# Performance work log

Measured on AMD Instinct MI355X. Metric: run time of the kernel, lower is better.

The kernel has to match this reference:

```python
import jax, jax.numpy as jnp
import numpy as np

INPUT_SIZE = 8
HIDDEN = 64


def setup_inputs() -> dict:
    key = jax.random.key(0)
    ks = jax.random.split(key, 7)
    B, T = 4096, 512
    s_ih = 1.0 / np.sqrt(HIDDEN)
    return {
        "input": jax.random.normal(ks[0], (B, T, INPUT_SIZE), dtype=jnp.float32),
        # PyTorch LSTM params: gate order i, f, g, o stacked along dim 0
        "W_ih": jax.random.uniform(ks[1], (4 * HIDDEN, INPUT_SIZE), minval=-s_ih, maxval=s_ih, dtype=jnp.float32),
        "W_hh": jax.random.uniform(ks[2], (4 * HIDDEN, HIDDEN), minval=-s_ih, maxval=s_ih, dtype=jnp.float32),
        "b_ih": jax.random.uniform(ks[3], (4 * HIDDEN,), minval=-s_ih, maxval=s_ih, dtype=jnp.float32),
        "b_hh": jax.random.uniform(ks[4], (4 * HIDDEN,), minval=-s_ih, maxval=s_ih, dtype=jnp.float32),
        "W_dense": jax.random.uniform(ks[5], (1, HIDDEN), minval=-s_ih, maxval=s_ih, dtype=jnp.float32),
        "b_dense": jax.random.uniform(ks[6], (1,), minval=-s_ih, maxval=s_ih, dtype=jnp.float32),
    }


def _lstm_seq(x, W_ih, W_hh, b_ih, b_hh):
    # x: [B, T, I] -> h_seq: [B, T, H]
    B = x.shape[0]
    # precompute input projections for all timesteps: [T, B, 4H]
    x_proj = jnp.einsum('bti,gi->tbg', x, W_ih) + (b_ih + b_hh)

    def step(carry, xp):
        h, c = carry
        gates = xp + h @ W_hh.T  # [B, 4H]
        i, f, g, o = jnp.split(gates, 4, axis=-1)
        i = jax.nn.sigmoid(i)
        f = jax.nn.sigmoid(f)
        g = jnp.tanh(g)
        o = jax.nn.sigmoid(o)
        c = f * c + i * g
        h = o * jnp.tanh(c)
        return (h, c), h

    h0 = jnp.zeros((B, HIDDEN), dtype=x.dtype)
    c0 = jnp.zeros((B, HIDDEN), dtype=x.dtype)
    _, h_seq = jax.lax.scan(step, (h0, c0), x_proj)  # [T, B, H]
    return jnp.transpose(h_seq, (1, 0, 2))  # [B, T, H]


def reference(input, W_ih, W_hh, b_ih, b_hh, W_dense, b_dense):
    h_t = _lstm_seq(input, W_ih, W_hh, b_ih, b_hh)  # [B, T, H]
    return h_t @ W_dense.T + b_dense  # [B, T, 1]
```

## Files before the change

### kernel.cpp

```cpp
#include <hip/hip_runtime.h>

#define T_SEQ 512
#define ISZ 8
#define HID 64
#define L2E 1.44269504088896340736f

typedef __bf16 bf16x8 __attribute__((ext_vector_type(8)));
typedef float  f32x4  __attribute__((ext_vector_type(4)));

__device__ __forceinline__ float exp2_hw(float x) {
    float r; asm("v_exp_f32 %0, %1" : "=v"(r) : "v"(x)); return r;
}
__device__ __forceinline__ unsigned cvt_pk_bf16(float a, float b) {
    unsigned r; asm("v_cvt_pk_bf16_f32 %0, %1, %2" : "=v"(r) : "v"(a), "v"(b)); return r;
}

__global__ __launch_bounds__(256, 2) void lstm_v7_kernel(
    const float* __restrict__ x,
    const float* __restrict__ W_ih,
    const float* __restrict__ W_hh,
    const float* __restrict__ b_ih,
    const float* __restrict__ b_hh,
    const float* __restrict__ W_dense,
    const float* __restrict__ b_dense,
    float* __restrict__ out)
{
    __shared__ __align__(16) __bf16 hpl[2][16 * 64];
    __shared__ __align__(16) __bf16 xs[2][160];
    __shared__ __align__(16) __bf16 xz[8];

    const int tid  = threadIdx.x;
    const int lane = tid & 63;
    const int w    = tid >> 6;
    const int q    = lane >> 4;
    const int sub  = lane & 15;
    const int br   = 2 * (sub >> 2) + (sub & 1);
    const bool isLo = (sub & 2) != 0;
    const long b0  = (long)blockIdx.x * 8;

    bf16x8 Bg[4][3];
    float biasg[4];
    #pragma unroll
    for (int g = 0; g < 4; ++g) {
        const int m = g * HID + 16 * w + sub;
        const float sc = (g == 2) ? (2.0f * L2E) : (-L2E);
        biasg[g] = (b_ih[m] + b_hh[m]) * sc;
        #pragma unroll
        for (int s = 0; s < 3; ++s) {
            #pragma unroll
            for (int e = 0; e < 8; ++e) {
                const int k = 32 * s + 8 * q + e;
                float v = 0.0f;
                if (k < HID)            v = W_hh[m * HID + k] * sc;
                else if (k < HID + ISZ) v = W_ih[m * ISZ + (k - HID)] * sc;
                Bg[g][s][e] = (__bf16)v;
            }
        }
    }
    f32x4 Cs[4];
    #pragma unroll
    for (int g = 0; g < 4; ++g) { Cs[g][0] = biasg[g]; Cs[g][1] = biasg[g]; Cs[g][2] = 0.f; Cs[g][3] = 0.f; }

    bf16x8 Bwd[2];
    #pragma unroll
    for (int s = 0; s < 2; ++s) {
        #pragma unroll
        for (int e = 0; e < 8; ++e) {
            const int k = 32 * s + 8 * q + e;
            const float wv = W_dense[k];
            const __bf16 whi = (__bf16)wv;
            float val = (sub == 0) ? (float)whi : (sub == 1) ? (wv - (float)whi) : 0.0f;
            Bwd[s][e] = (__bf16)val;
        }
    }

    for (int i = tid; i < 512; i += 256) ((float*)&hpl[1][0])[i] = 0.0f;
    if (tid < 4) ((float*)&xz[0])[tid] = 0.0f;

    const int  pr = lane >> 1, ph = lane & 1;
    const float* xbase = x + ((b0 + pr) * (long)T_SEQ) * ISZ + ph * 4;
    const int  xoffH = pr * 8 + ph * 4;
    const int  xoffL = 64 + xoffH;

    if (w == 3 && lane < 16) {
        float4 xv = *(const float4*)xbase;
        unsigned h01 = cvt_pk_bf16(xv.x, xv.y);
        unsigned h23 = cvt_pk_bf16(xv.z, xv.w);
        float f0 = __uint_as_float(h01 << 16), f1 = __uint_as_float(h01 & 0xffff0000u);
        float f2 = __uint_as_float(h23 << 16), f3 = __uint_as_float(h23 & 0xffff0000u);
        unsigned l01 = cvt_pk_bf16(xv.x - f0, xv.y - f1);
        unsigned l23 = cvt_pk_bf16(xv.z - f2, xv.w - f3);
        uint2 hh2; hh2.x = h01; hh2.y = h23;
        uint2 ll2; ll2.x = l01; ll2.y = l23;
        *(uint2*)&xs[0][xoffH] = hh2;
        *(uint2*)&xs[0][xoffL] = ll2;
    }

    const __bf16* xrd0 = (q == 0) ? &xs[0][(isLo ? 64 : 0) + br * 8] : &xz[0];
    const __bf16* xrd1 = (q == 0) ? &xs[1][(isLo ? 64 : 0) + br * 8] : &xz[0];

    float c0 = 0.f, c1 = 0.f;
    const float bd  = b_dense[0];
    const f32x4 Z   = {0.f, 0.f, 0.f, 0.f};
    const int  swz  = (sub & 7) << 3;
    const int  jme  = 16 * w + sub;

    float s0[4], s1[4];
    s0[0]=s0[1]=s0[2]=s0[3]=0.f;
    s1[0]=s1[1]=s1[2]=s1[3]=0.f;

    __syncthreads();

#define MF(A, B, C) __builtin_amdgcn_mfma_f32_16x16x32_bf16(A, B, C, 0, 0, 0)

#define STEP(P, PB, XR, XW)                                                          \
    {                                                                                \
        const int t = tb + P;                                                        \
                    \
        float4 xv;                                                                   \
        if (w == 3 && lane < 16) {                                                   \
            const int tn = (t + 1 < T_SEQ) ? (t + 1) : (T_SEQ - 1);                  \
            xv = *(const float4*)(xbase + (long)tn * ISZ);                           \
        }                                                                            \
            \
        bf16x8 Ax  = *(const bf16x8*)(XR);                                           \
        bf16x8 Ah0 = *(const bf16x8*)&hpl[PB][sub * 64 + ((8 * q)      ^ swz)];      \
        bf16x8 Ah1 = *(const bf16x8*)&hpl[PB][sub * 64 + ((32 + 8 * q) ^ swz)];      \
                                            \
        __builtin_amdgcn_s_setprio(1);                                               \
        f32x4 a0 = MF(Ax, Bg[0][2], Cs[0]);                                          \
        f32x4 a1 = MF(Ax, Bg[1][2], Cs[1]);                                          \
        f32x4 a2 = MF(Ax, Bg[2][2], Cs[2]);                                          \
        f32x4 a3 = MF(Ax, Bg[3][2], Cs[3]);                                          \
        a0 = MF(Ah0, Bg[0][0], a0); a0 = MF(Ah1, Bg[0][1], a0);                      \
        a1 = MF(Ah0, Bg[1][0], a1); a1 = MF(Ah1, Bg[1][1], a1);                      \
        a2 = MF(Ah0, Bg[2][0], a2); a2 = MF(Ah1, Bg[2][1], a2);                      \
        a3 = MF(Ah0, Bg[3][0], a3); a3 = MF(Ah1, Bg[3][1], a3);                      \
        __builtin_amdgcn_s_setprio(0);                                               \
                                 \
        if (w == 0) {                                                                \
            f32x4 oz = MF(Ah0, Bwd[0], Z);                                           \
            oz = MF(Ah1, Bwd[1], oz);                                                \
            float v0 = oz[0] + oz[2];                                                \
            float v1 = oz[1] + oz[3];                                                \
            v0 += __shfl_xor(v0, 1);                                                 \
            v1 += __shfl_xor(v1, 1);                                                 \
            s0[(P + 3) & 3] = v0;                                                    \
            s1[(P + 3) & 3] = v1;                                                    \
        }                                                                            \
                   \
        _Pragma("unroll")                                                            \
        for (int i = 0; i < 2; ++i) {                                                \
            const float gi = a0[i] + a0[2 + i];                                      \
            const float gf = a1[i] + a1[2 + i];                                      \
            const float gg = a2[i] + a2[2 + i];                                      \
            const float go = a3[i] + a3[2 + i];                                      \
            const float eA = exp2_hw(gi);                                            \
            const float eF = exp2_hw(gf);                                            \
            const float eB = exp2_hw(gg);                                            \
            const float ig = (eB - 1.0f) *                                           \
                __builtin_amdgcn_rcpf((1.0f + eA) * (1.0f + eB));                    \
            const float ff = __builtin_amdgcn_rcpf(1.0f + eF);                       \
            float cc = i ? c1 : c0;                                                  \
            cc = fmaf(ff, cc, ig);                                                   \
            if (i) c1 = cc; else c0 = cc;                                            \
            const float eO = exp2_hw(go);                                            \
            const float eC = exp2_hw(fminf(cc * (2.0f * L2E), 80.0f));               \
            const float hh = (eC - 1.0f) *                                           \
                __builtin_amdgcn_rcpf((1.0f + eO) * (1.0f + eC));                    \
            const __bf16 hi = (__bf16)hh;                                            \
            const __bf16 lo = (__bf16)(hh - (float)hi);                              \
            const int rh = 4 * q + i;                                                \
            const int rl = rh + 2;                                                   \
            hpl[PB ^ 1][rh * 64 + (jme ^ ((rh & 7) << 3))] = hi;                     \
            hpl[PB ^ 1][rl * 64 + (jme ^ ((rl & 7) << 3))] = lo;                     \
        }                                                                            \
               \
        if (w == 3 && lane < 16) {                                                   \
            unsigned h01 = cvt_pk_bf16(xv.x, xv.y);                                  \
            unsigned h23 = cvt_pk_bf16(xv.z, xv.w);                                  \
            float f0 = __uint_as_float(h01 << 16);                                   \
            float f1 = __uint_as_float(h01 & 0xffff0000u);                           \
            float f2 = __uint_as_float(h23 << 16);                                   \
            float f3 = __uint_as_float(h23 & 0xffff0000u);                           \
            unsigned l01 = cvt_pk_bf16(xv.x - f0, xv.y - f1);                        \
            unsigned l23 = cvt_pk_bf16(xv.z - f2, xv.w - f3);                        \
            uint2 hh2; hh2.x = h01; hh2.y = h23;                                     \
            uint2 ll2; ll2.x = l01; ll2.y = l23;                                     \
            *(uint2*)&xs[XW][xoffH] = hh2;                                           \
            *(uint2*)&xs[XW][xoffL] = ll2;                                           \
        }                                                                            \
                 \
        if (P == 0) {                                                                \
            if (w == 0 && sub == 0 && tb >= 4) {                                     \
                *(float4*)&out[(b0 + 2 * q) * T_SEQ + tb - 4] =                      \
                    make_float4(s0[0] + bd, s0[1] + bd, s0[2] + bd, s0[3] + bd);     \
                *(float4*)&out[(b0 + 2 * q + 1) * T_SEQ + tb - 4] =                  \
                    make_float4(s1[0] + bd, s1[1] + bd, s1[2] + bd, s1[3] + bd);     \
            }                                                                        \
        }                                                                            \
            \
        asm volatile("s_waitcnt lgkmcnt(0)" ::: "memory");                           \
        __builtin_amdgcn_s_barrier();                                                \
        __builtin_amdgcn_sched_barrier(0);                                           \
    }

    for (int tb = 0; tb < T_SEQ; tb += 4) {
        STEP(0, 1, xrd0, 1)
        STEP(1, 0, xrd1, 0)
        STEP(2, 1, xrd0, 1)
        STEP(3, 0, xrd1, 0)
    }
#undef STEP

    if (w == 0) {
        bf16x8 Eh0 = *(const bf16x8*)&hpl[1][sub * 64 + ((8 * q)      ^ swz)];
        bf16x8 Eh1 = *(const bf16x8*)&hpl[1][sub * 64 + ((32 + 8 * q) ^ swz)];
        f32x4 oz = MF(Eh0, Bwd[0], Z);
        oz = MF(Eh1, Bwd[1], oz);
        float v0 = oz[0] + oz[2];
        float v1 = oz[1] + oz[3];
        v0 += __shfl_xor(v0, 1);
        v1 += __shfl_xor(v1, 1);
        s0[3] = v0;
        s1[3] = v1;
        if (sub == 0) {
            *(float4*)&out[(b0 + 2 * q) * T_SEQ + (T_SEQ - 4)] =
                make_float4(s0[0] + bd, s0[1] + bd, s0[2] + bd, s0[3] + bd);
            *(float4*)&out[(b0 + 2 * q + 1) * T_SEQ + (T_SEQ - 4)] =
                make_float4(s1[0] + bd, s1[1] + bd, s1[2] + bd, s1[3] + bd);
        }
    }
#undef MF
}

extern "C" void kernel_launch(void* const* d_in, const int* in_sizes, int n_in,
                              void* d_out, int out_size, void* d_ws, size_t ws_size,
                              hipStream_t stream) {
    const float* x       = (const float*)d_in[0];
    const float* W_ih    = (const float*)d_in[1];
    const float* W_hh    = (const float*)d_in[2];
    const float* b_ih    = (const float*)d_in[3];
    const float* b_hh    = (const float*)d_in[4];
    const float* W_dense = (const float*)d_in[5];
    const float* b_dense = (const float*)d_in[6];
    float* out = (float*)d_out;

    const int B = in_sizes[0] / (T_SEQ * ISZ);
    const int blocks = B / 8;
    lstm_v7_kernel<<<blocks, 256, 0, stream>>>(x, W_ih, W_hh, b_ih, b_hh,
                                               W_dense, b_dense, out);
}
```

Before: 281.2 us.

## Interleave two independent 8-sequence LSTM groups per block for ILP

Each block now handles 16 batch rows as two independent groups (A and B), each with its own h ping-pong and x staging buffers. Their MFMA chains and activations are interleaved within each timestep, so one group's dependent MFMA latency and transcendental work can hide behind the other's, and the per-step barrier cost is shared across twice the work. Launch bounds drop to 1 block per CU and the grid halves to 256 blocks, which roughly matches CU count but lowers wave-level occupancy. Register pressure also roughly doubles for accumulators.

```diff
diff --git a/kernel.cpp b/kernel.cpp
--- a/kernel.cpp
+++ b/kernel.cpp
@@ -15,7 +15,7 @@
     unsigned r; asm("v_cvt_pk_bf16_f32 %0, %1, %2" : "=v"(r) : "v"(a), "v"(b)); return r;
 }
 
-__global__ __launch_bounds__(256, 2) void lstm_v7_kernel(
+__global__ __launch_bounds__(256, 1) void lstm_v8_kernel(
     const float* __restrict__ x,
     const float* __restrict__ W_ih,
     const float* __restrict__ W_hh,
@@ -25,8 +25,10 @@
     const float* __restrict__ b_dense,
     float* __restrict__ out)
 {
-    __shared__ __align__(16) __bf16 hpl[2][16 * 64];
-    __shared__ __align__(16) __bf16 xs[2][160];
+    __shared__ __align__(16) __bf16 hplA[2][16 * 64];
+    __shared__ __align__(16) __bf16 hplB[2][16 * 64];
+    __shared__ __align__(16) __bf16 xsA[2][160];
+    __shared__ __align__(16) __bf16 xsB[2][160];
     __shared__ __align__(16) __bf16 xz[8];
 
     const int tid  = threadIdx.x;
@@ -36,7 +38,7 @@
     const int sub  = lane & 15;
     const int br   = 2 * (sub >> 2) + (sub & 1);
     const bool isLo = (sub & 2) != 0;
-    const long b0  = (long)blockIdx.x * 8;
+    const long b0  = (long)blockIdx.x * 16;
 
     bf16x8 Bg[4][3];
     float biasg[4];
@@ -74,164 +76,209 @@
         }
     }
 
-    for (int i = tid; i < 512; i += 256) ((float*)&hpl[1][0])[i] = 0.0f;
+    for (int i = tid; i < 512; i += 256) {
+        ((float*)&hplA[1][0])[i] = 0.0f;
+        ((float*)&hplB[1][0])[i] = 0.0f;
+    }
     if (tid < 4) ((float*)&xz[0])[tid] = 0.0f;
 
     const int  pr = lane >> 1, ph = lane & 1;
-    const float* xbase = x + ((b0 + pr) * (long)T_SEQ) * ISZ + ph * 4;
+    const float* xbaseA = x + ((b0 + pr) * (long)T_SEQ) * ISZ + ph * 4;
+    const float* xbaseB = x + ((b0 + 8 + pr) * (long)T_SEQ) * ISZ + ph * 4;
     const int  xoffH = pr * 8 + ph * 4;
     const int  xoffL = 64 + xoffH;
 
-    if (w == 3 && lane < 16) {
-        float4 xv = *(const float4*)xbase;
-        unsigned h01 = cvt_pk_bf16(xv.x, xv.y);
-        unsigned h23 = cvt_pk_bf16(xv.z, xv.w);
-        float f0 = __uint_as_float(h01 << 16), f1 = __uint_as_float(h01 & 0xffff0000u);
-        float f2 = __uint_as_float(h23 << 16), f3 = __uint_as_float(h23 & 0xffff0000u);
-        unsigned l01 = cvt_pk_bf16(xv.x - f0, xv.y - f1);
-        unsigned l23 = cvt_pk_bf16(xv.z - f2, xv.w - f3);
-        uint2 hh2; hh2.x = h01; hh2.y = h23;
-        uint2 ll2; ll2.x = l01; ll2.y = l23;
-        *(uint2*)&xs[0][xoffH] = hh2;
-        *(uint2*)&xs[0][xoffL] = ll2;
-    }
-
-    const __bf16* xrd0 = (q == 0) ? &xs[0][(isLo ? 64 : 0) + br * 8] : &xz[0];
-    const __bf16* xrd1 = (q == 0) ? &xs[1][(isLo ? 64 : 0) + br * 8] : &xz[0];
-
-    float c0 = 0.f, c1 = 0.f;
+#define XWRITE(XV, DST)                                                      \
+    {                                                                        \
+        unsigned h01 = cvt_pk_bf16(XV.x, XV.y);                              \
+        unsigned h23 = cvt_pk_bf16(XV.z, XV.w);                              \
+        float f0 = __uint_as_float(h01 << 16);                               \
+        float f1 = __uint_as_float(h01 & 0xffff0000u);                       \
+        float f2 = __uint_as_float(h23 << 16);                               \
+        float f3 = __uint_as_float(h23 & 0xffff0000u);                       \
+        unsigned l01 = cvt_pk_bf16(XV.x - f0, XV.y - f1);                    \
+        unsigned l23 = cvt_pk_bf16(XV.z - f2, XV.w - f3);                    \
+        uint2 hh2; hh2.x = h01; hh2.y = h23;                                 \
+        uint2 ll2; ll2.x = l01; ll2.y = l23;                                 \
+        *(uint2*)&(DST)[xoffH] = hh2;                                        \
+        *(uint2*)&(DST)[xoffL] = ll2;                                        \
+    }
+
+    if (w == 3 && lane < 16) { float4 xv = *(const float4*)xbaseA; XWRITE(xv, &xsA[0][0]) }
+    if (w == 2 && lane < 16) { float4 xv = *(const float4*)xbaseB; XWRITE(xv, &xsB[0][0]) }
+
+    const __bf16* xrdA0 = (q == 0) ? &xsA[0][(isLo ? 64 : 0) + br * 8] : &xz[0];
+    const __bf16* xrdA1 = (q == 0) ? &xsA[1][(isLo ? 64 : 0) + br * 8] : &xz[0];
+    const __bf16* xrdB0 = (q == 0) ? &xsB[0][(isLo ? 64 : 0) + br * 8] : &xz[0];
+    const __bf16* xrdB1 = (q == 0) ? &xsB[1][(isLo ? 64 : 0) + br * 8] : &xz[0];
+
+    float cA0 = 0.f, cA1 = 0.f, cB0 = 0.f, cB1 = 0.f;
     const float bd  = b_dense[0];
     const f32x4 Z   = {0.f, 0.f, 0.f, 0.f};
     const int  swz  = (sub & 7) << 3;
     const int  jme  = 16 * w + sub;
 
-    float s0[4], s1[4];
-    s0[0]=s0[1]=s0[2]=s0[3]=0.f;
-    s1[0]=s1[1]=s1[2]=s1[3]=0.f;
+    float s0A[4], s1A[4], s0B[4], s1B[4];
+    #pragma unroll
+    for (int i = 0; i < 4; ++i) { s0A[i] = 0.f; s1A[i] = 0.f; s0B[i] = 0.f; s1B[i] = 0.f; }
 
     __syncthreads();
 
 #define MF(A, B, C) __builtin_amdgcn_mfma_f32_16x16x32_bf16(A, B, C, 0, 0, 0)
 
-#define STEP(P, PB, XR, XW)                                                          \
-    {                                                                                \
-        const int t = tb + P;                                                        \
-                    \
-        float4 xv;                                                                   \
-        if (w == 3 && lane < 16) {                                                   \
-            const int tn = (t + 1 < T_SEQ) ? (t + 1) : (T_SEQ - 1);                  \
-            xv = *(const float4*)(xbase + (long)tn * ISZ);                           \
-        }                                                                            \
-            \
-        bf16x8 Ax  = *(const bf16x8*)(XR);                                           \
-        bf16x8 Ah0 = *(const bf16x8*)&hpl[PB][sub * 64 + ((8 * q)      ^ swz)];      \
-        bf16x8 Ah1 = *(const bf16x8*)&hpl[PB][sub * 64 + ((32 + 8 * q) ^ swz)];      \
-                                            \
-        __builtin_amdgcn_s_setprio(1);                                               \
-        f32x4 a0 = MF(Ax, Bg[0][2], Cs[0]);                                          \
-        f32x4 a1 = MF(Ax, Bg[1][2], Cs[1]);                                          \
-        f32x4 a2 = MF(Ax, Bg[2][2], Cs[2]);                                          \
-        f32x4 a3 = MF(Ax, Bg[3][2], Cs[3]);                                          \
-        a0 = MF(Ah0, Bg[0][0], a0); a0 = MF(Ah1, Bg[0][1], a0);                      \
-        a1 = MF(Ah0, Bg[1][0], a1); a1 = MF(Ah1, Bg[1][1], a1);                      \
-        a2 = MF(Ah0, Bg[2][0], a2); a2 = MF(Ah1, Bg[2][1], a2);                      \
-        a3 = MF(Ah0, Bg[3][0], a3); a3 = MF(Ah1, Bg[3][1], a3);                      \
-        __builtin_amdgcn_s_setprio(0);                                               \
-                                 \
-        if (w == 0) {                                                                \
-            f32x4 oz = MF(Ah0, Bwd[0], Z);                                           \
-            oz = MF(Ah1, Bwd[1], oz);                                                \
-            float v0 = oz[0] + oz[2];                                                \
-            float v1 = oz[1] + oz[3];                                                \
-            v0 += __shfl_xor(v0, 1);                                                 \
-            v1 += __shfl_xor(v1, 1);                                                 \
-            s0[(P + 3) & 3] = v0;                                                    \
-            s1[(P + 3) & 3] = v1;                                                    \
-        }                                                                            \
-                   \
-        _Pragma("unroll")                                                            \
-        for (int i = 0; i < 2; ++i) {                                                \
-            const float gi = a0[i] + a0[2 + i];                                      \
-            const float gf = a1[i] + a1[2 + i];                                      \
-            const float gg = a2[i] + a2[2 + i];                                      \
-            const float go = a3[i] + a3[2 + i];                                      \
-            const float eA = exp2_hw(gi);                                            \
-            const float eF = exp2_hw(gf);                                            \
-            const float eB = exp2_hw(gg);                                            \
-            const float ig = (eB - 1.0f) *                                           \
-                __builtin_amdgcn_rcpf((1.0f + eA) * (1.0f + eB));                    \
-            const float ff = __builtin_amdgcn_rcpf(1.0f + eF);                       \
-            float cc = i ? c1 : c0;                                                  \
-            cc = fmaf(ff, cc, ig);                                                   \
-            if (i) c1 = cc; else c0 = cc;                                            \
-            const float eO = exp2_hw(go);                                            \
-            const float eC = exp2_hw(fminf(cc * (2.0f * L2E), 80.0f));               \
-            const float hh = (eC - 1.0f) *                                           \
-                __builtin_amdgcn_rcpf((1.0f + eO) * (1.0f + eC));                    \
-            const __bf16 hi = (__bf16)hh;                                            \
-            const __bf16 lo = (__bf16)(hh - (float)hi);                              \
-            const int rh = 4 * q + i;                                                \
-            const int rl = rh + 2;                                                   \
-            hpl[PB ^ 1][rh * 64 + (jme ^ ((rh & 7) << 3))] = hi;                     \
-            hpl[PB ^ 1][rl * 64 + (jme ^ ((rl & 7) << 3))] = lo;                     \
-        }                                                                            \
-               \
-        if (w == 3 && lane < 16) {                                                   \
-            unsigned h01 = cvt_pk_bf16(xv.x, xv.y);                                  \
-            unsigned h23 = cvt_pk_bf16(xv.z, xv.w);                                  \
-            float f0 = __uint_as_float(h01 << 16);                                   \
-            float f1 = __uint_as_float(h01 & 0xffff0000u);                           \
-            float f2 = __uint_as_float(h23 << 16);                                   \
-            float f3 = __uint_as_float(h23 & 0xffff0000u);                           \
-            unsigned l01 = cvt_pk_bf16(xv.x - f0, xv.y - f1);                        \
-            unsigned l23 = cvt_pk_bf16(xv.z - f2, xv.w - f3);                        \
-            uint2 hh2; hh2.x = h01; hh2.y = h23;                                     \
-            uint2 ll2; ll2.x = l01; ll2.y = l23;                                     \
-            *(uint2*)&xs[XW][xoffH] = hh2;                                           \
-            *(uint2*)&xs[XW][xoffL] = ll2;                                           \
-        }                                                                            \
-                 \
-        if (P == 0) {                                                                \
-            if (w == 0 && sub == 0 && tb >= 4) {                                     \
-                *(float4*)&out[(b0 + 2 * q) * T_SEQ + tb - 4] =                      \
-                    make_float4(s0[0] + bd, s0[1] + bd, s0[2] + bd, s0[3] + bd);     \
-                *(float4*)&out[(b0 + 2 * q + 1) * T_SEQ + tb - 4] =                  \
-                    make_float4(s1[0] + bd, s1[1] + bd, s1[2] + bd, s1[3] + bd);     \
-            }                                                                        \
-        }                                                                            \
-            \
-        asm volatile("s_waitcnt lgkmcnt(0)" ::: "memory");                           \
-        __builtin_amdgcn_s_barrier();                                                \
-        __builtin_amdgcn_sched_barrier(0);                                           \
+#define ACT(A0, A1, A2, A3, CC0, CC1, HW)                                    \
+    _Pragma("unroll")                                                        \
+    for (int i = 0; i < 2; ++i) {                                            \
+        const float gi = A0[i] + A0[2 + i];                                  \
+        const float gf = A1[i] + A1[2 + i];                                  \
+        const float gg = A2[i] + A2[2 + i];                                  \
+        const float go = A3[i] + A3[2 + i];                                  \
+        const float eA = exp2_hw(gi);                                        \
+        const float eF = exp2_hw(gf);                                        \
+        const float eB = exp2_hw(gg);                                        \
+        const float ig = (eB - 1.0f) *                                       \
+            __builtin_amdgcn_rcpf((1.0f + eA) * (1.0f + eB));                \
+        const float ff = __builtin_amdgcn_rcpf(1.0f + eF);                   \
+        float cc = i ? CC1 : CC0;                                            \
+        cc = fmaf(ff, cc, ig);                                               \
+        if (i) CC1 = cc; else CC0 = cc;                                      \
+        const float eO = exp2_hw(go);                                        \
+        const float eC = exp2_hw(fminf(cc * (2.0f * L2E), 80.0f));           \
+        const float hh = (eC - 1.0f) *                                       \
+            __builtin_amdgcn_rcpf((1.0f + eO) * (1.0f + eC));                \
+        const __bf16 hi = (__bf16)hh;                                        \
+        const __bf16 lo = (__bf16)(hh - (float)hi);                          \
+        const int rh = 4 * q + i;                                            \
+        const int rl = rh + 2;                                               \
+        (HW)[rh * 64 + (jme ^ ((rh & 7) << 3))] = hi;                        \
+        (HW)[rl * 64 + (jme ^ ((rl & 7) << 3))] = lo;                        \
+    }
+
+#define DENSE(AH0, AH1, S0, S1, PP)                                          \
+    {                                                                        \
+        f32x4 oz = MF(AH0, Bwd[0], Z);                                       \
+        oz = MF(AH1, Bwd[1], oz);                                            \
+        float v0 = oz[0] + oz[2];                                            \
+        float v1 = oz[1] + oz[3];                                            \
+        v0 += __shfl_xor(v0, 1);                                             \
+        v1 += __shfl_xor(v1, 1);                                             \
+        (S0)[((PP) + 3) & 3] = v0;                                           \
+        (S1)[((PP) + 3) & 3] = v1;                                           \
+    }
+
+#define STEP(P, PB, XRA, XRB, XW)                                            \
+    {                                                                        \
+        const int t = tb + P;                                                \
+        float4 xvA, xvB;                                                     \
+        if (w == 3 && lane < 16) {                                           \
+            const int tn = (t + 1 < T_SEQ) ? (t + 1) : (T_SEQ - 1);          \
+            xvA = *(const float4*)(xbaseA + (long)tn * ISZ);                 \
+        }                                                                    \
+        if (w == 2 && lane < 16) {                                           \
+            const int tn = (t + 1 < T_SEQ) ? (t + 1) : (T_SEQ - 1);          \
+            xvB = *(const float4*)(xbaseB + (long)tn * ISZ);                 \
+        }                                                                    \
+        bf16x8 AxA  = *(const bf16x8*)(XRA);                                 \
+        bf16x8 AxB  = *(const bf16x8*)(XRB);                                 \
+        bf16x8 AhA0 = *(const bf16x8*)&hplA[PB][sub * 64 + ((8 * q)      ^ swz)]; \
+        bf16x8 AhA1 = *(const bf16x8*)&hplA[PB][sub * 64 + ((32 + 8 * q) ^ swz)]; \
+        bf16x8 AhB0 = *(const bf16x8*)&hplB[PB][sub * 64 + ((8 * q)      ^ swz)]; \
+        bf16x8 AhB1 = *(const bf16x8*)&hplB[PB][sub * 64 + ((32 + 8 * q) ^ swz)]; \
+        __builtin_amdgcn_s_setprio(1);                                       \
+        f32x4 aA0 = MF(AxA, Bg[0][2], Cs[0]);                                \
+        f32x4 aB0 = MF(AxB, Bg[0][2], Cs[0]);                                \
+        f32x4 aA1 = MF(AxA, Bg[1][2], Cs[1]);                                \
+        f32x4 aB1 = MF(AxB, Bg[1][2], Cs[1]);                                \
+        f32x4 aA2 = MF(AxA, Bg[2][2], Cs[2]);                                \
+        f32x4 aB2 = MF(AxB, Bg[2][2], Cs[2]);                                \
+        f32x4 aA3 = MF(AxA, Bg[3][2], Cs[3]);                                \
+        f32x4 aB3 = MF(AxB, Bg[3][2], Cs[3]);                                \
+        aA0 = MF(AhA0, Bg[0][0], aA0); aB0 = MF(AhB0, Bg[0][0], aB0);        \
+        aA1 = MF(AhA0, Bg[1][0], aA1); aB1 = MF(AhB0, Bg[1][0], aB1);        \
+        aA2 = MF(AhA0, Bg[2][0], aA2); aB2 = MF(AhB0, Bg[2][0], aB2);        \
+        aA3 = MF(AhA0, Bg[3][0], aA3); aB3 = MF(AhB0, Bg[3][0], aB3);        \
+        aA0 = MF(AhA1, Bg[0][1], aA0); aB0 = MF(AhB1, Bg[0][1], aB0);        \
+        aA1 = MF(AhA1, Bg[1][1], aA1); aB1 = MF(AhB1, Bg[1][1], aB1);        \
+        aA2 = MF(AhA1, Bg[2][1], aA2); aB2 = MF(AhB1, Bg[2][1], aB2);        \
+        aA3 = MF(AhA1, Bg[3][1], aA3); aB3 = MF(AhB1, Bg[3][1], aB3);        \
+        __builtin_amdgcn_s_setprio(0);                                       \
+                     \
+        if (w == 0) DENSE(AhA0, AhA1, s0A, s1A, P)                           \
+        if (w == 1) DENSE(AhB0, AhB1, s0B, s1B, P)                           \
+          \
+        ACT(aA0, aA1, aA2, aA3, cA0, cA1, &hplA[PB ^ 1][0])                  \
+        ACT(aB0, aB1, aB2, aB3, cB0, cB1, &hplB[PB ^ 1][0])                  \
+         \
+        if (w == 3 && lane < 16) XWRITE(xvA, &xsA[XW][0])                    \
+        if (w == 2 && lane < 16) XWRITE(xvB, &xsB[XW][0])                    \
+        \
+        if (P == 0 && tb >= 4) {                                             \
+            if (w == 0 && sub == 0) {                                        \
+                *(float4*)&out[(b0 + 2 * q) * T_SEQ + tb - 4] =              \
+                    make_float4(s0A[0] + bd, s0A[1] + bd, s0A[2] + bd, s0A[3] + bd); \
+                *(float4*)&out[(b0 + 2 * q + 1) * T_SEQ + tb - 4] =          \
+                    make_float4(s1A[0] + bd, s1A[1] + bd, s1A[2] + bd, s1A[3] + bd); \
+            }                                                                \
+            if (w == 1 && sub == 0) {                                        \
+                *(float4*)&out[(b0 + 8 + 2 * q) * T_SEQ + tb - 4] =          \
+                    make_float4(s0B[0] + bd, s0B[1] + bd, s0B[2] + bd, s0B[3] + bd); \
+                *(float4*)&out[(b0 + 8 + 2 * q + 1) * T_SEQ + tb - 4] =      \
+                    make_float4(s1B[0] + bd, s1B[1] + bd, s1B[2] + bd, s1B[3] + bd); \
+            }                                                                \
+        }                                                                    \
+        asm volatile("s_waitcnt lgkmcnt(0)" ::: "memory");                   \
+        __builtin_amdgcn_s_barrier();                                        \
+        __builtin_amdgcn_sched_barrier(0);                                   \
     }
 
     for (int tb = 0; tb < T_SEQ; tb += 4) {
-        STEP(0, 1, xrd0, 1)
-        STEP(1, 0, xrd1, 0)
-        STEP(2, 1, xrd0, 1)
-        STEP(3, 0, xrd1, 0)
+        STEP(0, 1, xrdA0, xrdB0, 1)
+        STEP(1, 0, xrdA1, xrdB1, 0)
+        STEP(2, 1, xrdA0, xrdB0, 1)
+        STEP(3, 0, xrdA1, xrdB1, 0)
     }
 #undef STEP
 
     if (w == 0) {
-        bf16x8 Eh0 = *(const bf16x8*)&hpl[1][sub * 64 + ((8 * q)      ^ swz)];
-        bf16x8 Eh1 = *(const bf16x8*)&hpl[1][sub * 64 + ((32 + 8 * q) ^ swz)];
+        bf16x8 Eh0 = *(const bf16x8*)&hplA[1][sub * 64 + ((8 * q)      ^ swz)];
+        bf16x8 Eh1 = *(const bf16x8*)&hplA[1][sub * 64 + ((32 + 8 * q) ^ swz)];
         f32x4 oz = MF(Eh0, Bwd[0], Z);
         oz = MF(Eh1, Bwd[1], oz);
         float v0 = oz[0] + oz[2];
         float v1 = oz[1] + oz[3];
         v0 += __shfl_xor(v0, 1);
         v1 += __shfl_xor(v1, 1);
-        s0[3] = v0;
-        s1[3] = v1;
+        s0A[3] = v0;
+        s1A[3] = v1;
         if (sub == 0) {
             *(float4*)&out[(b0 + 2 * q) * T_SEQ + (T_SEQ - 4)] =
-                make_float4(s0[0] + bd, s0[1] + bd, s0[2] + bd, s0[3] + bd);
+                make_float4(s0A[0] + bd, s0A[1] + bd, s0A[2] + bd, s0A[3] + bd);
             *(float4*)&out[(b0 + 2 * q + 1) * T_SEQ + (T_SEQ - 4)] =
-                make_float4(s1[0] + bd, s1[1] + bd, s1[2] + bd, s1[3] + bd);
+                make_float4(s1A[0] + bd, s1A[1] + bd, s1A[2] + bd, s1A[3] + bd);
         }
     }
+    if (w == 1) {
+        bf16x8 Eh0 = *(const bf16x8*)&hplB[1][sub * 64 + ((8 * q)      ^ swz)];
+        bf16x8 Eh1 = *(const bf16x8*)&hplB[1][sub * 64 + ((32 + 8 * q) ^ swz)];
+        f32x4 oz = MF(Eh0, Bwd[0], Z);
+        oz = MF(Eh1, Bwd[1], oz);
+        float v0 = oz[0] + oz[2];
+        float v1 = oz[1] + oz[3];
+        v0 += __shfl_xor(v0, 1);
+        v1 += __shfl_xor(v1, 1);
+        s0B[3] = v0;
+        s1B[3] = v1;
+        if (sub == 0) {
+            *(float4*)&out[(b0 + 8 + 2 * q) * T_SEQ + (T_SEQ - 4)] =
+                make_float4(s0B[0] + bd, s0B[1] + bd, s0B[2] + bd, s0B[3] + bd);
+            *(float4*)&out[(b0 + 8 + 2 * q + 1) * T_SEQ + (T_SEQ - 4)] =
+                make_float4(s1B[0] + bd, s1B[1] + bd, s1B[2] + bd, s1B[3] + bd);
+        }
+    }
 #undef MF
+#undef ACT
+#undef DENSE
+#undef XWRITE
 }
 
 extern "C" void kernel_launch(void* const* d_in, const int* in_sizes, int n_in,
@@ -247,7 +294,7 @@
     float* out = (float*)d_out;
 
     const int B = in_sizes[0] / (T_SEQ * ISZ);
-    const int blocks = B / 8;
-    lstm_v7_kernel<<<blocks, 256, 0, stream>>>(x, W_ih, W_hh, b_ih, b_hh,
+    const int blocks = B / 16;
+    lstm_v8_kernel<<<blocks, 256, 0, stream>>>(x, W_ih, W_hh, b_ih, b_hh,
                                                W_dense, b_dense, out);
 }
```

Measured after the change: 389.3 us. +38.4%, slower.

## Halve batch rows per block to double block count and occupancy

Applied to the files above, without the earlier changes.

Each block now handles 4 batch rows instead of 8. The MFMA tile layout is remapped so each lane processes one row pair (hi/lo split) instead of two, the x staging buffer is shrunk, and launch bounds are raised to 4 blocks per SIMD group. The aim is to shorten per-step latency in the serial recurrence and spread work over twice as many blocks, so more of the GPU is busy and latency is hidden. In exchange, MFMA utilisation per block drops (half the tile rows are idle) and total MFMA work doubles.

```diff
diff --git a/kernel.cpp b/kernel.cpp
--- a/kernel.cpp
+++ b/kernel.cpp
@@ -15,7 +15,7 @@
     unsigned r; asm("v_cvt_pk_bf16_f32 %0, %1, %2" : "=v"(r) : "v"(a), "v"(b)); return r;
 }
 
-__global__ __launch_bounds__(256, 2) void lstm_v7_kernel(
+__global__ __launch_bounds__(256, 4) void lstm_v9_kernel(
     const float* __restrict__ x,
     const float* __restrict__ W_ih,
     const float* __restrict__ W_hh,
@@ -26,7 +26,7 @@
     float* __restrict__ out)
 {
     __shared__ __align__(16) __bf16 hpl[2][16 * 64];
-    __shared__ __align__(16) __bf16 xs[2][160];
+    __shared__ __align__(16) __bf16 xs[2][80];
     __shared__ __align__(16) __bf16 xz[8];
 
     const int tid  = threadIdx.x;
@@ -34,9 +34,7 @@
     const int w    = tid >> 6;
     const int q    = lane >> 4;
     const int sub  = lane & 15;
-    const int br   = 2 * (sub >> 2) + (sub & 1);
-    const bool isLo = (sub & 2) != 0;
-    const long b0  = (long)blockIdx.x * 8;
+    const long b0  = (long)blockIdx.x * 4;
 
     bf16x8 Bg[4][3];
     float biasg[4];
@@ -59,7 +57,7 @@
     }
     f32x4 Cs[4];
     #pragma unroll
-    for (int g = 0; g < 4; ++g) { Cs[g][0] = biasg[g]; Cs[g][1] = biasg[g]; Cs[g][2] = 0.f; Cs[g][3] = 0.f; }
+    for (int g = 0; g < 4; ++g) { Cs[g][0] = biasg[g]; Cs[g][1] = 0.f; Cs[g][2] = 0.f; Cs[g][3] = 0.f; }
 
     bf16x8 Bwd[2];
     #pragma unroll
@@ -74,40 +72,45 @@
         }
     }
 
-    for (int i = tid; i < 512; i += 256) ((float*)&hpl[1][0])[i] = 0.0f;
+    for (int i = tid; i < 1024; i += 256) ((float*)&hpl[0][0])[i] = 0.0f;
     if (tid < 4) ((float*)&xz[0])[tid] = 0.0f;
 
     const int  pr = lane >> 1, ph = lane & 1;
     const float* xbase = x + ((b0 + pr) * (long)T_SEQ) * ISZ + ph * 4;
     const int  xoffH = pr * 8 + ph * 4;
-    const int  xoffL = 64 + xoffH;
-
-    if (w == 3 && lane < 16) {
-        float4 xv = *(const float4*)xbase;
-        unsigned h01 = cvt_pk_bf16(xv.x, xv.y);
-        unsigned h23 = cvt_pk_bf16(xv.z, xv.w);
-        float f0 = __uint_as_float(h01 << 16), f1 = __uint_as_float(h01 & 0xffff0000u);
-        float f2 = __uint_as_float(h23 << 16), f3 = __uint_as_float(h23 & 0xffff0000u);
-        unsigned l01 = cvt_pk_bf16(xv.x - f0, xv.y - f1);
-        unsigned l23 = cvt_pk_bf16(xv.z - f2, xv.w - f3);
-        uint2 hh2; hh2.x = h01; hh2.y = h23;
-        uint2 ll2; ll2.x = l01; ll2.y = l23;
-        *(uint2*)&xs[0][xoffH] = hh2;
-        *(uint2*)&xs[0][xoffL] = ll2;
-    }
-
-    const __bf16* xrd0 = (q == 0) ? &xs[0][(isLo ? 64 : 0) + br * 8] : &xz[0];
-    const __bf16* xrd1 = (q == 0) ? &xs[1][(isLo ? 64 : 0) + br * 8] : &xz[0];
-
-    float c0 = 0.f, c1 = 0.f;
+    const int  xoffL = 32 + xoffH;
+
+#define XWRITE(XV, DST)                                                      \
+    {                                                                        \
+        unsigned h01 = cvt_pk_bf16(XV.x, XV.y);                              \
+        unsigned h23 = cvt_pk_bf16(XV.z, XV.w);                              \
+        float f0 = __uint_as_float(h01 << 16);                               \
+        float f1 = __uint_as_float(h01 & 0xffff0000u);                       \
+        float f2 = __uint_as_float(h23 << 16);                               \
+        float f3 = __uint_as_float(h23 & 0xffff0000u);                       \
+        unsigned l01 = cvt_pk_bf16(XV.x - f0, XV.y - f1);                    \
+        unsigned l23 = cvt_pk_bf16(XV.z - f2, XV.w - f3);                    \
+        uint2 hh2; hh2.x = h01; hh2.y = h23;                                 \
+        uint2 ll2; ll2.x = l01; ll2.y = l23;                                 \
+        *(uint2*)&(DST)[xoffH] = hh2;                                        \
+        *(uint2*)&(DST)[xoffL] = ll2;                                        \
+    }
+
+    if (w == 3 && lane < 8) { float4 xv = *(const float4*)xbase; XWRITE(xv, &xs[0][0]) }
+
+    const bool xvalid = (q == 0) && !(sub & 2);
+    const int  xoff   = ((sub & 1) ? 32 : 0) + (sub >> 2) * 8;
+    const __bf16* xrd0 = xvalid ? &xs[0][xoff] : &xz[0];
+    const __bf16* xrd1 = xvalid ? &xs[1][xoff] : &xz[0];
+
+    float c0 = 0.f;
     const float bd  = b_dense[0];
     const f32x4 Z   = {0.f, 0.f, 0.f, 0.f};
     const int  swz  = (sub & 7) << 3;
     const int  jme  = 16 * w + sub;
 
-    float s0[4], s1[4];
+    float s0[4];
     s0[0]=s0[1]=s0[2]=s0[3]=0.f;
-    s1[0]=s1[1]=s1[2]=s1[3]=0.f;
 
     __syncthreads();
 
@@ -118,7 +121,7 @@
         const int t = tb + P;                                                        \
                     \
         float4 xv;                                                                   \
-        if (w == 3 && lane < 16) {                                                   \
+        if (w == 3 && lane < 8) {                                                    \
             const int tn = (t + 1 < T_SEQ) ? (t + 1) : (T_SEQ - 1);                  \
             xv = *(const float4*)(xbase + (long)tn * ISZ);                           \
         }                                                                            \
@@ -141,62 +144,41 @@
         if (w == 0) {                                                                \
             f32x4 oz = MF(Ah0, Bwd[0], Z);                                           \
             oz = MF(Ah1, Bwd[1], oz);                                                \
-            float v0 = oz[0] + oz[2];                                                \
-            float v1 = oz[1] + oz[3];                                                \
+            float v0 = oz[0] + oz[1];                                                \
             v0 += __shfl_xor(v0, 1);                                                 \
-            v1 += __shfl_xor(v1, 1);                                                 \
             s0[(P + 3) & 3] = v0;                                                    \
-            s1[(P + 3) & 3] = v1;                                                    \
-        }                                                                            \
-                   \
-        _Pragma("unroll")                                                            \
-        for (int i = 0; i < 2; ++i) {                                                \
-            const float gi = a0[i] + a0[2 + i];                                      \
-            const float gf = a1[i] + a1[2 + i];                                      \
-            const float gg = a2[i] + a2[2 + i];                                      \
-            const float go = a3[i] + a3[2 + i];                                      \
+        }                                                                            \
+                    \
+        {                                                                            \
+            const float gi = a0[0] + a0[1];                                          \
+            const float gf = a1[0] + a1[1];                                          \
+            const float gg = a2[0] + a2[1];                                          \
+            const float go = a3[0] + a3[1];                                          \
             const float eA = exp2_hw(gi);                                            \
             const float eF = exp2_hw(gf);                                            \
             const float eB = exp2_hw(gg);                                            \
             const float ig = (eB - 1.0f) *                                           \
                 __builtin_amdgcn_rcpf((1.0f + eA) * (1.0f + eB));                    \
             const float ff = __builtin_amdgcn_rcpf(1.0f + eF);                       \
-            float cc = i ? c1 : c0;                                                  \
-            cc = fmaf(ff, cc, ig);                                                   \
-            if (i) c1 = cc; else c0 = cc;                                            \
+            c0 = fmaf(ff, c0, ig);                                                   \
             const float eO = exp2_hw(go);                                            \
-            const float eC = exp2_hw(fminf(cc * (2.0f * L2E), 80.0f));               \
+            const float eC = exp2_hw(fminf(c0 * (2.0f * L2E), 80.0f));               \
             const float hh = (eC - 1.0f) *                                           \
                 __builtin_amdgcn_rcpf((1.0f + eO) * (1.0f + eC));                    \
             const __bf16 hi = (__bf16)hh;                                            \
             const __bf16 lo = (__bf16)(hh - (float)hi);                              \
-            const int rh = 4 * q + i;                                                \
-            const int rl = rh + 2;                                                   \
+            const int rh = 4 * q;                                                    \
+            const int rl = rh + 1;                                                   \
             hpl[PB ^ 1][rh * 64 + (jme ^ ((rh & 7) << 3))] = hi;                     \
             hpl[PB ^ 1][rl * 64 + (jme ^ ((rl & 7) << 3))] = lo;                     \
         }                                                                            \
                \
-        if (w == 3 && lane < 16) {                                                   \
-            unsigned h01 = cvt_pk_bf16(xv.x, xv.y);                                  \
-            unsigned h23 = cvt_pk_bf16(xv.z, xv.w);                                  \
-            float f0 = __uint_as_float(h01 << 16);                                   \
-            float f1 = __uint_as_float(h01 & 0xffff0000u);                           \
-            float f2 = __uint_as_float(h23 << 16);                                   \
-            float f3 = __uint_as_float(h23 & 0xffff0000u);                           \
-            unsigned l01 = cvt_pk_bf16(xv.x - f0, xv.y - f1);                        \
-            unsigned l23 = cvt_pk_bf16(xv.z - f2, xv.w - f3);                        \
-            uint2 hh2; hh2.x = h01; hh2.y = h23;                                     \
-            uint2 ll2; ll2.x = l01; ll2.y = l23;                                     \
-            *(uint2*)&xs[XW][xoffH] = hh2;                                           \
-            *(uint2*)&xs[XW][xoffL] = ll2;                                           \
-        }                                                                            \
+        if (w == 3 && lane < 8) XWRITE(xv, &xs[XW][0])                               \
                  \
         if (P == 0) {                                                                \
             if (w == 0 && sub == 0 && tb >= 4) {                                     \
-                *(float4*)&out[(b0 + 2 * q) * T_SEQ + tb - 4] =                      \
+                *(float4*)&out[(b0 + q) * T_SEQ + tb - 4] =                          \
                     make_float4(s0[0] + bd, s0[1] + bd, s0[2] + bd, s0[3] + bd);     \
-                *(float4*)&out[(b0 + 2 * q + 1) * T_SEQ + tb - 4] =                  \
-                    make_float4(s1[0] + bd, s1[1] + bd, s1[2] + bd, s1[3] + bd);     \
             }                                                                        \
         }                                                                            \
             \
@@ -218,20 +200,16 @@
         bf16x8 Eh1 = *(const bf16x8*)&hpl[1][sub * 64 + ((32 + 8 * q) ^ swz)];
         f32x4 oz = MF(Eh0, Bwd[0], Z);
         oz = MF(Eh1, Bwd[1], oz);
-        float v0 = oz[0] + oz[2];
-        float v1 = oz[1] + oz[3];
+        float v0 = oz[0] + oz[1];
         v0 += __shfl_xor(v0, 1);
-        v1 += __shfl_xor(v1, 1);
         s0[3] = v0;
-        s1[3] = v1;
         if (sub == 0) {
-            *(float4*)&out[(b0 + 2 * q) * T_SEQ + (T_SEQ - 4)] =
+            *(float4*)&out[(b0 + q) * T_SEQ + (T_SEQ - 4)] =
                 make_float4(s0[0] + bd, s0[1] + bd, s0[2] + bd, s0[3] + bd);
-            *(float4*)&out[(b0 + 2 * q + 1) * T_SEQ + (T_SEQ - 4)] =
-                make_float4(s1[0] + bd, s1[1] + bd, s1[2] + bd, s1[3] + bd);
         }
     }
 #undef MF
+#undef XWRITE
 }
 
 extern "C" void kernel_launch(void* const* d_in, const int* in_sizes, int n_in,
@@ -247,7 +225,7 @@
     float* out = (float*)d_out;
 
     const int B = in_sizes[0] / (T_SEQ * ISZ);
-    const int blocks = B / 8;
-    lstm_v7_kernel<<<blocks, 256, 0, stream>>>(x, W_ih, W_hh, b_ih, b_hh,
+    const int blocks = B / 4;
+    lstm_v9_kernel<<<blocks, 256, 0, stream>>>(x, W_ih, W_hh, b_ih, b_hh,
                                                W_dense, b_dense, out);
 }
```

Result: slower. 511.8 us (+82.0%).
